# Optimization experiments

Measured on AMD Instinct MI355X. Metric: run time of the kernel, lower is better.

The kernel has to match this reference:

```python
import jax, jax.numpy as jnp
import numpy as np

Q = 127.0  # int8 symmetric quantization range


def _round_ste(v):
    # straight-through rounding (forward: round; backward: identity)
    return v + jax.lax.stop_gradient(jnp.round(v) - v)


def quantize_rowwise(x):
    # per-row absmax int8 quantization: returns int8-valued float tensor + row scale
    absmax = jnp.max(jnp.abs(x), axis=1, keepdims=True)  # [N,1]
    q = jnp.clip(_round_ste(x * (Q / absmax)), -Q, Q)
    return q, absmax


def quantize_global(w):
    # whole-tensor absmax int8 quantization
    absmax = jnp.max(jnp.abs(w))
    q = jnp.clip(_round_ste(w * (Q / absmax)), -Q, Q)
    return q, absmax


def int8_matmul_dequant_bias(a_q, b_q_t, state_a, state_b, bias):
    # a_q: [N,K] int8-valued, b_q_t: [K,M]; dequant = state_a*state_b/(127*127)
    acc = jnp.matmul(a_q, b_q_t)  # int8-valued floats -> exact small-int products
    return acc * (state_a * state_b / (Q * Q)) + bias


def setup_inputs() -> dict:
    key = jax.random.key(0)
    k1, k2, k3, k4, k5 = jax.random.split(key, 5)
    B, S, D, H = 4, 2048, 2048, 8192
    x = jax.random.normal(k1, (B, S, D), dtype=jnp.float32)
    W1 = jax.random.normal(k2, (H, D), dtype=jnp.float32) * (1.0 / np.sqrt(D))
    B1 = jax.random.normal(k3, (H,), dtype=jnp.float32) * 0.02
    W2 = jax.random.normal(k4, (D, H), dtype=jnp.float32) * (1.0 / np.sqrt(H))
    B2 = jax.random.normal(k5, (D,), dtype=jnp.float32) * 0.02
    return {"x": x, "W1": W1, "B1": B1, "W2": W2, "B2": B2}


def reference(x, W1, B1, W2, B2):
    X1 = x.reshape(-1, x.shape[-1])  # [N, D]
    X1_q, sX1 = quantize_rowwise(X1)
    W1_q, sW1 = quantize_global(W1)
    X2_pre = int8_matmul_dequant_bias(X1_q, W1_q.T, sX1, sW1, B1)  # [N, H]
    X2 = jax.nn.gelu(X2_pre, approximate=True)  # fused gelu in original kernel
    X2_q, sX2 = quantize_rowwise(X2)
    W2_q, sW2 = quantize_global(W2)
    out = int8_matmul_dequant_bias(X2_q, W2_q.T, sX2, sW2, B2)  # [N, D]
    return out.reshape(*x.shape[:-1], -1)
```

## Files before the change

kernel.cpp:

```cpp
#include <hip/hip_runtime.h>
#include <cstdint>
#include <cstddef>


typedef int v4i __attribute__((ext_vector_type(4)));

#define AS1 __attribute__((address_space(1)))
#define AS3 __attribute__((address_space(3)))

#define WAIT_LGKM(N) asm volatile("s_waitcnt lgkmcnt(" #N ")" ::: "memory")
#define WAIT_VM(N)   asm volatile("s_waitcnt vmcnt(" #N ")" ::: "memory")
#define SBAR() __builtin_amdgcn_s_barrier()
#define SFENCE() __builtin_amdgcn_sched_barrier(0)

__device__ __forceinline__ void gload_lds16(const void* g, void* l) {
    __builtin_amdgcn_global_load_lds((const AS1 void*)g, (AS3 void*)l, 16, 0, 0);
}

__device__ __forceinline__ float absmax4(float4 v, float cur) {
    return fmaxf(cur, fmaxf(fmaxf(fabsf(v.x), fabsf(v.y)),
                            fmaxf(fabsf(v.z), fabsf(v.w))));
}

__device__ __forceinline__ int quant1(float x, float inv) {
    int q = (int)rintf(x * inv);
    return min(127, max(-127, q));
}

__device__ __forceinline__ uint32_t quant4(float4 v, float inv) {
    uint32_t b0 = (uint32_t)(uint8_t)(int8_t)quant1(v.x, inv);
    uint32_t b1 = (uint32_t)(uint8_t)(int8_t)quant1(v.y, inv);
    uint32_t b2 = (uint32_t)(uint8_t)(int8_t)quant1(v.z, inv);
    uint32_t b3 = (uint32_t)(uint8_t)(int8_t)quant1(v.w, inv);
    return b0 | (b1 << 8) | (b2 << 16) | (b3 << 24);
}

__global__ __launch_bounds__(256) void wabs_kernel(
    const float* __restrict__ W, int n4, float* __restrict__ out)
{
    int tid = blockIdx.x * 256 + threadIdx.x;
    int stride = gridDim.x * 256;
    const float4* W4 = (const float4*)W;
    float amax = 0.0f;
    for (int i = tid; i < n4; i += stride) amax = absmax4(W4[i], amax);
    #pragma unroll
    for (int off = 32; off >= 1; off >>= 1)
        amax = fmaxf(amax, __shfl_xor(amax, off));
    __shared__ float red[4];
    if ((threadIdx.x & 63) == 0) red[threadIdx.x >> 6] = amax;
    __syncthreads();
    if (threadIdx.x == 0) {
        amax = fmaxf(fmaxf(red[0], red[1]), fmaxf(red[2], red[3]));
        atomicMax((int*)out, __float_as_int(amax));
    }
}

__global__ __launch_bounds__(256) void wquant_kernel(
    const float* __restrict__ W, int n4, const float* __restrict__ s,
    uint32_t* __restrict__ Wq)
{
    float inv = 127.0f / s[0];
    int tid = blockIdx.x * 256 + threadIdx.x;
    int stride = gridDim.x * 256;
    const float4* W4 = (const float4*)W;
    for (int i = tid; i < n4; i += stride) Wq[i] = quant4(W4[i], inv);
}

template<int CNT>
__global__ __launch_bounds__(256) void rowquant_kernel(
    const float* __restrict__ X, int8_t* __restrict__ Xq,
    float* __restrict__ rowAbs)
{
    const int row = blockIdx.x;
    const int t = threadIdx.x;
    const size_t cols = (size_t)CNT * 1024;
    const float4* Xr = (const float4*)(X + (size_t)row * cols);
    float4 vals[CNT];
    float amax = 0.0f;
    #pragma unroll
    for (int j = 0; j < CNT; j++) {
        vals[j] = Xr[j * 256 + t];
        amax = absmax4(vals[j], amax);
    }
    #pragma unroll
    for (int off = 32; off >= 1; off >>= 1)
        amax = fmaxf(amax, __shfl_xor(amax, off));
    __shared__ float red[4];
    if ((t & 63) == 0) red[t >> 6] = amax;
    __syncthreads();
    amax = fmaxf(fmaxf(red[0], red[1]), fmaxf(red[2], red[3]));
    if (t == 0) rowAbs[row] = amax;
    float inv = 127.0f / amax;
    uint32_t* out = (uint32_t*)(Xq + (size_t)row * cols);
    #pragma unroll
    for (int j = 0; j < CNT; j++) out[j * 256 + t] = quant4(vals[j], inv);
}

template<int GELU>
__global__ __launch_bounds__(512, 2) void gemm8_i8(
    const int8_t* __restrict__ A, const int8_t* __restrict__ B,
    int K, int Ncols, int nbx,
    const float* __restrict__ rowScale, const float* __restrict__ wScale,
    const float* __restrict__ bias, float* __restrict__ Cout)
{
    extern __shared__ int8_t lds[];
    int8_t* AsB = lds;
    int8_t* BsB = lds + 65536;

    const int nwg = gridDim.x;
    const int bid = blockIdx.x;
    const int wg = (bid & 7) * (nwg >> 3) + (bid >> 3);
    const int bx = wg % nbx;
    const int by = wg / nbx;
    const int brow = by * 256;
    const int bcol = bx * 256;

    const int t = threadIdx.x;
    const int lane = t & 63;
    const int w = t >> 6;
    const int wr = w >> 2;
    const int wc = w & 3;
    const int llo = lane & 15;
    const int lhi = lane >> 4;

    const int8_t* gA = A + (size_t)brow * K;
    const int8_t* gB = B + (size_t)bcol * K;

    const size_t srcOffBase = (size_t)(t >> 2) * K
                            + (size_t)(((t & 3) ^ ((t >> 3) & 3)) * 16);
    const int ldsDst = t * 16;

    const int sA = ((lhi ^ ((llo >> 1) & 3)) << 4);
    const int aOff = (wr * 128 + llo) * 64 + sA;
    const int bOff = (wc * 64 + llo) * 64 + sA;

    const int NT = K >> 6;

    v4i acc[8][4] = {};

    auto stageA = [&](int srcTile) {
        const size_t gb = (size_t)srcTile * 64 + srcOffBase;
        int8_t* d = AsB + (srcTile & 3) * 16384 + ldsDst;
        gload_lds16(gA + gb, d);
        gload_lds16(gA + gb + (size_t)128 * K, d + 8192);
    };
    auto stageB = [&](int srcTile) {
        const size_t gb = (size_t)srcTile * 64 + srcOffBase;
        int8_t* d = BsB + (srcTile & 3) * 16384 + ldsDst;
        gload_lds16(gB + gb, d);
        gload_lds16(gB + gb + (size_t)128 * K, d + 8192);
    };

    stageA(0); stageB(0); stageA(1); stageB(1); stageA(2); stageB(2);
    WAIT_VM(8);
    SFENCE();
    SBAR();

    #define MFMA16(AV, BV, MOFF)                                            \
        __builtin_amdgcn_s_setprio(1);                                      \
        _Pragma("unroll")                                                   \
        for (int m = 0; m < 4; m++)                                         \
            _Pragma("unroll")                                               \
            for (int n = 0; n < 4; n++)                                     \
                acc[MOFF + m][n] = __builtin_amdgcn_mfma_i32_16x16x64_i8(   \
                    AV[m], BV[n], acc[MOFF + m][n], 0, 0, 0);               \
        __builtin_amdgcn_s_setprio(0);

    for (int T = 0; T < NT; ++T) {
        const int buf = T & 3;
        const int8_t* Ab = AsB + buf * 16384;
        const int8_t* Bb = BsB + buf * 16384;
        const int ts = (T + 3 < NT) ? T + 3 : NT - 1;
        v4i a0[4], a1[4], bb[4];

        #pragma unroll
        for (int m = 0; m < 4; m++) a0[m] = *(const v4i*)(Ab + aOff + m * 1024);
        #pragma unroll
        for (int n = 0; n < 4; n++) bb[n] = *(const v4i*)(Bb + bOff + n * 1024);
        stageA(ts);
        SBAR();
        WAIT_LGKM(0);
        SFENCE();
        MFMA16(a0, bb, 0)
        SBAR();

        #pragma unroll
        for (int m = 0; m < 4; m++) a1[m] = *(const v4i*)(Ab + aOff + 4096 + m * 1024);
        stageB(ts);
        SBAR();
        WAIT_LGKM(0);
        SFENCE();
        MFMA16(a1, bb, 4)
        WAIT_VM(8);
        SFENCE();
        SBAR();
    }
    #undef MFMA16

    WAIT_VM(0);

    const float wsc = wScale[0] * (1.0f / (127.0f * 127.0f));
    #pragma unroll
    for (int m = 0; m < 8; m++) {
        #pragma unroll
        for (int r4 = 0; r4 < 4; r4++) {
            const int row = brow + wr * 128 + m * 16 + lhi * 4 + r4;
            const float s = rowScale[row] * wsc;
            #pragma unroll
            for (int n = 0; n < 4; n++) {
                const int col = bcol + wc * 64 + n * 16 + llo;
                float v = (float)acc[m][n][r4] * s + bias[col];
                if (GELU) {
                    float u = v + 0.044715f * v * v * v;
                    v = v / (1.0f + __expf(-1.5957691216057308f * u));
                }
                Cout[(size_t)row * Ncols + col] = v;
            }
        }
    }
}

extern "C" void kernel_launch(void* const* d_in, const int* in_sizes, int n_in,
                              void* d_out, int out_size, void* d_ws, size_t ws_size,
                              hipStream_t stream)
{
    const float* x  = (const float*)d_in[0];
    const float* W1 = (const float*)d_in[1];
    const float* B1 = (const float*)d_in[2];
    const float* W2 = (const float*)d_in[3];
    const float* B2 = (const float*)d_in[4];
    float* out = (float*)d_out;

    const int N = 8192, D = 2048, H = 8192;
    const size_t MB = 1024 * 1024;

    hipFuncSetAttribute((const void*)gemm8_i8<1>,
                        hipFuncAttributeMaxDynamicSharedMemorySize, 131072);
    hipFuncSetAttribute((const void*)gemm8_i8<0>,
                        hipFuncAttributeMaxDynamicSharedMemorySize, 131072);

    char* ws = (char*)d_ws;
    float* sW1 = (float*)(ws + 0);
    float* sW2 = (float*)(ws + 4);
    float* sX1 = (float*)(ws + 256);
    float* sX2 = (float*)(ws + 256 + 32768);
    size_t off = 1 * MB;
    int8_t* X1q = (int8_t*)(ws + off);
    int8_t* W2q = X1q;
    off += (size_t)N * D;
    int8_t* W1q = (int8_t*)(ws + off); off += (size_t)H * D;
    int8_t* X2q = (int8_t*)(ws + off); off += (size_t)N * H;
    float*  X2f = (float*)(ws + off);
    const size_t fixedBytes = off;

    int chunk = N;
    if (ws_size < fixedBytes + (size_t)N * H * 4) {
        size_t avail = ws_size > fixedBytes ? ws_size - fixedBytes : 0;
        size_t c = avail / ((size_t)H * 4);
        c = (c / 256) * 256;
        if (c < 256) c = 256;
        if (c > (size_t)N) c = N;
        chunk = (int)c;
    }

    hipMemsetAsync(d_ws, 0, 256 + 65536, stream);

    wabs_kernel<<<2048, 256, 0, stream>>>(W1, H * D / 4, sW1);
    wquant_kernel<<<4096, 256, 0, stream>>>(W1, H * D / 4, sW1, (uint32_t*)W1q);
    rowquant_kernel<2><<<N, 256, 0, stream>>>(x, X1q, sX1);

    for (int r0 = 0; r0 < N; r0 += chunk) {
        const int rows = min(chunk, N - r0);
        gemm8_i8<1><<<(H / 256) * (rows / 256), 512, 131072, stream>>>(
            X1q + (size_t)r0 * D, W1q, D, H, H / 256,
            sX1 + r0, sW1, B1, X2f);
        rowquant_kernel<8><<<rows, 256, 0, stream>>>(
            X2f, X2q + (size_t)r0 * H, sX2 + r0);
    }

    wabs_kernel<<<2048, 256, 0, stream>>>(W2, D * H / 4, sW2);
    wquant_kernel<<<4096, 256, 0, stream>>>(W2, D * H / 4, sW2, (uint32_t*)W2q);

    gemm8_i8<0><<<(D / 256) * (N / 256), 512, 131072, stream>>>(
        X2q, W2q, H, D, D / 256, sX2, sW2, B2, out);
}
```

Measured before the change: 628.0 us.

## Restructure int8 GEMM main loop into 3-stage ring with register prefetch

Rewrites the GEMM main loop to use a 3-buffer LDS ring (96 KB instead of 128 KB) and to issue both A and B global-to-LDS loads at the top of each iteration. Next-tile fragments are read from LDS into registers while the current MFMAs run, which removes one barrier per iteration. It also replaces the workgroup-to-tile mapping with a per-XCD column-chunk layout, using a shift parameter chosen per GEMM. The aim is better overlap of LDS reads with MFMA and better L2 locality per XCD. The trade-offs are higher register pressure from holding full A/B fragments, and a mapping that assumes the grid dimensions divide evenly.

```diff
diff --git a/kernel.cpp b/kernel.cpp
--- a/kernel.cpp
+++ b/kernel.cpp
@@ -99,19 +99,20 @@
 template<int GELU>
 __global__ __launch_bounds__(512, 2) void gemm8_i8(
     const int8_t* __restrict__ A, const int8_t* __restrict__ B,
-    int K, int Ncols, int nbx,
+    int K, int Ncols, int cs,
     const float* __restrict__ rowScale, const float* __restrict__ wScale,
     const float* __restrict__ bias, float* __restrict__ Cout)
 {
     extern __shared__ int8_t lds[];
     int8_t* AsB = lds;
-    int8_t* BsB = lds + 65536;
-
-    const int nwg = gridDim.x;
+    int8_t* BsB = lds + 49152;
+
     const int bid = blockIdx.x;
-    const int wg = (bid & 7) * (nwg >> 3) + (bid >> 3);
-    const int bx = wg % nbx;
-    const int by = wg / nbx;
+    const int c = bid & 7;
+    const int i = bid >> 3;
+    const int cpx = 1 << cs;
+    const int bx = c * cpx + (i & (cpx - 1));
+    const int by = i >> cs;
     const int brow = by * 256;
     const int bcol = bx * 256;
 
@@ -138,66 +139,60 @@
 
     v4i acc[8][4] = {};
 
-    auto stageA = [&](int srcTile) {
-        const size_t gb = (size_t)srcTile * 64 + srcOffBase;
-        int8_t* d = AsB + (srcTile & 3) * 16384 + ldsDst;
+    auto stageA = [&](int tile, int r) {
+        const size_t gb = (size_t)tile * 64 + srcOffBase;
+        int8_t* d = AsB + r * 16384 + ldsDst;
         gload_lds16(gA + gb, d);
         gload_lds16(gA + gb + (size_t)128 * K, d + 8192);
     };
-    auto stageB = [&](int srcTile) {
-        const size_t gb = (size_t)srcTile * 64 + srcOffBase;
-        int8_t* d = BsB + (srcTile & 3) * 16384 + ldsDst;
+    auto stageB = [&](int tile, int r) {
+        const size_t gb = (size_t)tile * 64 + srcOffBase;
+        int8_t* d = BsB + r * 16384 + ldsDst;
         gload_lds16(gB + gb, d);
         gload_lds16(gB + gb + (size_t)128 * K, d + 8192);
     };
 
-    stageA(0); stageB(0); stageA(1); stageB(1); stageA(2); stageB(2);
-    WAIT_VM(8);
+    stageA(0, 0); stageB(0, 0); stageA(1, 1); stageB(1, 1); stageA(2, 2); stageB(2, 2);
+    WAIT_VM(4);
     SFENCE();
     SBAR();
 
-    #define MFMA16(AV, BV, MOFF)                                            \
-        __builtin_amdgcn_s_setprio(1);                                      \
-        _Pragma("unroll")                                                   \
-        for (int m = 0; m < 4; m++)                                         \
-            _Pragma("unroll")                                               \
-            for (int n = 0; n < 4; n++)                                     \
-                acc[MOFF + m][n] = __builtin_amdgcn_mfma_i32_16x16x64_i8(   \
-                    AV[m], BV[n], acc[MOFF + m][n], 0, 0, 0);               \
-        __builtin_amdgcn_s_setprio(0);
-
+    v4i a[8], b[4];
+    #pragma unroll
+    for (int m = 0; m < 8; m++) a[m] = *(const v4i*)(AsB + aOff + m * 1024);
+    #pragma unroll
+    for (int n = 0; n < 4; n++) b[n] = *(const v4i*)(BsB + bOff + n * 1024);
+    WAIT_LGKM(0);
+    SFENCE();
+    SBAR();
+
+    int rT = 0;
     for (int T = 0; T < NT; ++T) {
-        const int buf = T & 3;
-        const int8_t* Ab = AsB + buf * 16384;
-        const int8_t* Bb = BsB + buf * 16384;
-        const int ts = (T + 3 < NT) ? T + 3 : NT - 1;
-        v4i a0[4], a1[4], bb[4];
+        if (T + 3 < NT) { stageA(T + 3, rT); stageB(T + 3, rT); }
+        const int rn = (rT + 1 < 3) ? rT + 1 : 0;
+        const int rb = (T + 1 < NT) ? rn : rT;
+        const int8_t* Ab = AsB + rb * 16384;
+        const int8_t* Bb = BsB + rb * 16384;
 
         #pragma unroll
-        for (int m = 0; m < 4; m++) a0[m] = *(const v4i*)(Ab + aOff + m * 1024);
+        for (int m = 0; m < 8; m++) {
+            __builtin_amdgcn_s_setprio(1);
+            #pragma unroll
+            for (int n = 0; n < 4; n++)
+                acc[m][n] = __builtin_amdgcn_mfma_i32_16x16x64_i8(
+                    a[m], b[n], acc[m][n], 0, 0, 0);
+            __builtin_amdgcn_s_setprio(0);
+            a[m] = *(const v4i*)(Ab + aOff + m * 1024);
+        }
         #pragma unroll
-        for (int n = 0; n < 4; n++) bb[n] = *(const v4i*)(Bb + bOff + n * 1024);
-        stageA(ts);
-        SBAR();
+        for (int n = 0; n < 4; n++) b[n] = *(const v4i*)(Bb + bOff + n * 1024);
+
         WAIT_LGKM(0);
-        SFENCE();
-        MFMA16(a0, bb, 0)
-        SBAR();
-
-        #pragma unroll
-        for (int m = 0; m < 4; m++) a1[m] = *(const v4i*)(Ab + aOff + 4096 + m * 1024);
-        stageB(ts);
-        SBAR();
-        WAIT_LGKM(0);
-        SFENCE();
-        MFMA16(a1, bb, 4)
-        WAIT_VM(8);
+        WAIT_VM(4);
         SFENCE();
         SBAR();
-    }
-    #undef MFMA16
-
-    WAIT_VM(0);
+        rT = rn;
+    }
 
     const float wsc = wScale[0] * (1.0f / (127.0f * 127.0f));
     #pragma unroll
@@ -235,9 +230,9 @@
     const size_t MB = 1024 * 1024;
 
     hipFuncSetAttribute((const void*)gemm8_i8<1>,
-                        hipFuncAttributeMaxDynamicSharedMemorySize, 131072);
+                        hipFuncAttributeMaxDynamicSharedMemorySize, 98304);
     hipFuncSetAttribute((const void*)gemm8_i8<0>,
-                        hipFuncAttributeMaxDynamicSharedMemorySize, 131072);
+                        hipFuncAttributeMaxDynamicSharedMemorySize, 98304);
 
     char* ws = (char*)d_ws;
     float* sW1 = (float*)(ws + 0);
@@ -271,8 +266,8 @@
 
     for (int r0 = 0; r0 < N; r0 += chunk) {
         const int rows = min(chunk, N - r0);
-        gemm8_i8<1><<<(H / 256) * (rows / 256), 512, 131072, stream>>>(
-            X1q + (size_t)r0 * D, W1q, D, H, H / 256,
+        gemm8_i8<1><<<(H / 256) * (rows / 256), 512, 98304, stream>>>(
+            X1q + (size_t)r0 * D, W1q, D, H, 2,
             sX1 + r0, sW1, B1, X2f);
         rowquant_kernel<8><<<rows, 256, 0, stream>>>(
             X2f, X2q + (size_t)r0 * H, sX2 + r0);
@@ -281,6 +276,6 @@
     wabs_kernel<<<2048, 256, 0, stream>>>(W2, D * H / 4, sW2);
     wquant_kernel<<<4096, 256, 0, stream>>>(W2, D * H / 4, sW2, (uint32_t*)W2q);
 
-    gemm8_i8<0><<<(D / 256) * (N / 256), 512, 131072, stream>>>(
-        X2q, W2q, H, D, D / 256, sX2, sW2, B2, out);
-}
+    gemm8_i8<0><<<(D / 256) * (N / 256), 512, 98304, stream>>>(
+        X2q, W2q, H, D, 0, sX2, sW2, B2, out);
+}
```

Result: slower. 654.4 us (+4.2%).
